# Kernel optimization log

Measured on AMD Instinct MI355X. Metric: run time of the kernel, lower is better.

The kernel has to match this reference:

```python
import jax, jax.numpy as jnp
import numpy as np


def _rms(x, w=None, eps=1e-6):
    # RMSNorm in fp32 like the torch module, optional elementwise affine.
    x32 = x.astype(jnp.float32)
    r = jax.lax.rsqrt(jnp.mean(x32 * x32, axis=-1, keepdims=True) + eps)
    y = (x32 * r).astype(x.dtype)
    return y * w if w is not None else y


def _rotate_half(x):
    x1, x2 = jnp.split(x, 2, axis=-1)
    return jnp.concatenate([-x2, x1], axis=-1)


def setup_inputs() -> dict:
    key = jax.random.key(0)
    ks = jax.random.split(key, 10)
    B, N, C, H = 16, 1024, 1152, 16
    hd = C // H          # 72
    hid = 3072           # _swiglu_hidden(1152, 4.0)
    grid = 32            # grid**2 == N
    quarter = hd // 4    # 18
    # exact axial RoPE cache (build_axial_rope_cache)
    inv_freq = 1.0 / (10000.0 ** (np.arange(quarter, dtype=np.float32) / quarter))
    pos = np.arange(grid, dtype=np.float32)
    f1 = pos[:, None] * inv_freq[None, :]                               # (grid, quarter)
    fy = np.broadcast_to(f1[:, None, :], (grid, grid, quarter)).reshape(-1, quarter)
    fx = np.broadcast_to(f1[None, :, :], (grid, grid, quarter)).reshape(-1, quarter)

    def cs(f):
        e = np.concatenate([f, f], axis=-1)                             # (N, hd//2)
        return jnp.asarray(np.cos(e))[None, None], jnp.asarray(np.sin(e))[None, None]

    cos_y, sin_y = cs(fy)
    cos_x, sin_x = cs(fx)

    def w(k, shp, scale=0.02):
        return jax.random.normal(k, shp, jnp.float32) * scale

    return {
        "x": jax.random.normal(ks[0], (B, N, C), jnp.float32),
        "temb": jax.random.normal(ks[1], (B, C), jnp.float32),
        "cos_y": cos_y, "sin_y": sin_y, "cos_x": cos_x, "sin_x": sin_x,
        "Wqkv": w(ks[2], (3 * C, C)), "bqkv": jnp.zeros((3 * C,), jnp.float32),
        "Wt": w(ks[3], (3 * C, C)), "bt": jnp.zeros((3 * C,), jnp.float32),
        "Wp": w(ks[4], (C, C)), "bp": jnp.zeros((C,), jnp.float32),
        "qn_w": jnp.ones((hd,), jnp.float32), "kn_w": jnp.ones((hd,), jnp.float32),
        "Wg": w(ks[5], (hid, C)), "bg": jnp.zeros((hid,), jnp.float32),
        "Wu": w(ks[6], (hid, C)), "bu": jnp.zeros((hid,), jnp.float32),
        "Wd": w(ks[7], (C, hid)), "bd": jnp.zeros((C,), jnp.float32),
    }


def reference(x, temb, cos_y, sin_y, cos_x, sin_x, Wqkv, bqkv, Wt, bt, Wp, bp,
              qn_w, kn_w, Wg, bg, Wu, bu, Wd, bd):
    B, N, C = x.shape
    H = 16
    hd = C // H

    # --- TMSA attention branch ---
    xn = _rms(x)                                            # norm1 (no affine)
    qkv = xn @ Wqkv.T + bqkv + (temb @ Wt.T + bt)[:, None, :]
    qkv = qkv.reshape(B, N, 3, H, hd).transpose(2, 0, 3, 1, 4)  # (3,B,H,N,hd)
    q, k, v = qkv[0], qkv[1], qkv[2]
    q = _rms(q, qn_w)
    k = _rms(k, kn_w)

    def rope(t):
        ty, tx = jnp.split(t, 2, axis=-1)
        ty = ty * cos_y + _rotate_half(ty) * sin_y
        tx = tx * cos_x + _rotate_half(tx) * sin_x
        return jnp.concatenate([ty, tx], axis=-1)

    q, k = rope(q), rope(k)

    scores = jnp.einsum('bhnd,bhmd->bhnm', q, k) / jnp.sqrt(jnp.float32(hd))
    attn = jax.nn.softmax(scores, axis=-1)
    o = jnp.einsum('bhnm,bhmd->bhnd', attn, v)
    o = o.transpose(0, 2, 1, 3).reshape(B, N, C)
    x = x + (o @ Wp.T + bp)

    # --- SwiGLU MLP branch ---
    xn2 = _rms(x)                                           # norm2 (no affine)
    h = jax.nn.silu(xn2 @ Wg.T + bg) * (xn2 @ Wu.T + bu)
    x = x + (h @ Wd.T + bd)
    return x
```

## Files before the change

### kernel.cpp

```cpp
#include <hip/hip_runtime.h>
#include <cstdint>
#include <cstddef>

typedef unsigned short u16;
typedef unsigned int u32;
typedef __attribute__((ext_vector_type(8))) short bf16x8s;
typedef __attribute__((ext_vector_type(4))) float f32x4;

__device__ __forceinline__ u16 f2bf(float f){
  union { float f; unsigned u; } v; v.f = f;
  unsigned r = v.u + 0x7FFFu + ((v.u >> 16) & 1u);
  return (u16)(r >> 16);
}
__device__ __forceinline__ float bf2f(u16 h){
  union { unsigned u; float f; } v; v.u = ((unsigned)h) << 16;
  return v.f;
}

__global__ __launch_bounds__(256) void cvt_kernel(const float* __restrict__ in,
                                                  u16* __restrict__ out, int n){
  int i = blockIdx.x*256 + threadIdx.x;
  if (i < n) out[i] = f2bf(in[i]);
}

__global__ __launch_bounds__(256) void cvt_gu_kernel(const float* __restrict__ Wg,
                                                     const float* __restrict__ Wu,
                                                     u16* __restrict__ out){
  size_t i = (size_t)blockIdx.x*256 + threadIdx.x;
  if (i >= (size_t)6144*1152) return;
  int j = (int)(i / 1152), k = (int)(i % 1152);
  int b16 = j >> 4, w = j & 15;
  int src = (b16 >> 1)*16 + w;
  const float* W = (b16 & 1) ? Wu : Wg;
  out[i] = f2bf(W[(size_t)src*1152 + k]);
}

__global__ __launch_bounds__(256) void temb_kernel(const float* __restrict__ temb,
                                                   const float* __restrict__ Wt,
                                                   const float* __restrict__ bt,
                                                   const float* __restrict__ bqkv,
                                                   float* __restrict__ tvec){
  int idx = blockIdx.x*256 + threadIdx.x;
  if (idx >= 16*3456) return;
  int b = idx / 3456, col = idx % 3456;
  const float* tp = temb + (size_t)b*1152;
  const float* wp = Wt + (size_t)col*1152;
  float s = 0.f;
  for (int k=0;k<1152;k++) s += tp[k]*wp[k];
  tvec[idx] = s + bt[col] + bqkv[col];
}

__global__ __launch_bounds__(256) void rms_kernel(const float* __restrict__ in,
                                                  u16* __restrict__ out, int C){
  int row = blockIdx.x;
  const float* p = in + (size_t)row*C;
  float ss = 0.f;
  for (int c = threadIdx.x; c < C; c += 256){ float v = p[c]; ss += v*v; }
  #pragma unroll
  for (int d=1; d<64; d<<=1) ss += __shfl_xor(ss, d);
  __shared__ float wsum[4];
  if ((threadIdx.x & 63) == 0) wsum[threadIdx.x>>6] = ss;
  __syncthreads();
  float tot = wsum[0]+wsum[1]+wsum[2]+wsum[3];
  float r = rsqrtf(tot/(float)C + 1e-6f);
  u16* o = out + (size_t)row*C;
  for (int c = threadIdx.x; c < C; c += 256) o[c] = f2bf(p[c]*r);
}

template<int MODE>
__global__ __launch_bounds__(256, 3) void gemm_kernel(
    const u16* __restrict__ A, const u16* __restrict__ B,
    int M, int N, int K, int nbx, int segw,
    const float* __restrict__ bias, const float* __restrict__ fextra,
    void* __restrict__ outv, u16* __restrict__ out2, u16* __restrict__ out3)
{
  __shared__ __align__(16) u16 As0[128*32];
  __shared__ __align__(16) u16 Bs0[128*32];
  __shared__ __align__(16) u16 As1[128*32];
  __shared__ __align__(16) u16 Bs1[128*32];
  __shared__ __align__(16) u16 As2[128*32];
  __shared__ __align__(16) u16 Bs2[128*32];
  const int tid  = threadIdx.x;
  const int lane = tid & 63;
  const int wv   = tid >> 6;
  const int wr   = wv >> 1, wc = wv & 1;

  const int nwg  = (int)gridDim.x;
  const int bid  = (int)blockIdx.x;
  const int xcd  = bid & 7;
  const int slot = bid >> 3;
  const int mdep = (nwg >> 3) / nbx;
  const int segsz = mdep * segw;
  const int seg  = slot / segsz;
  const int rem  = slot - seg*segsz;
  const int mi   = rem / segw;
  const int ni   = seg*segw + (rem - mi*segw);
  const long m0 = (long)(xcd*mdep + mi) * 128;
  const long n0 = (long)ni * 128;

  const u16* Ab = A + (size_t)m0*K;
  const u16* Bb = B + (size_t)n0*K;
  const int srow = tid >> 2;
  const int spos = (tid & 3) * 8;

  f32x4 acc[4][4];
  #pragma unroll
  for (int i=0;i<4;i++)
    #pragma unroll
    for (int j=0;j<4;j++) acc[i][j] = (f32x4){0.f,0.f,0.f,0.f};

  auto stage = [&](u16* as, u16* bs, int kt){
    __builtin_amdgcn_global_load_lds(
      (const __attribute__((address_space(1))) void*)(Ab + (size_t)srow*K + kt + spos),
      (__attribute__((address_space(3))) void*)(as + wv*512), 16, 0, 0);
    __builtin_amdgcn_global_load_lds(
      (const __attribute__((address_space(1))) void*)(Ab + (size_t)(64+srow)*K + kt + spos),
      (__attribute__((address_space(3))) void*)(as + 2048 + wv*512), 16, 0, 0);
    __builtin_amdgcn_global_load_lds(
      (const __attribute__((address_space(1))) void*)(Bb + (size_t)srow*K + kt + spos),
      (__attribute__((address_space(3))) void*)(bs + wv*512), 16, 0, 0);
    __builtin_amdgcn_global_load_lds(
      (const __attribute__((address_space(1))) void*)(Bb + (size_t)(64+srow)*K + kt + spos),
      (__attribute__((address_space(3))) void*)(bs + 2048 + wv*512), 16, 0, 0);
  };
  auto compute = [&](const u16* as, const u16* bs){
    const int kb = (lane>>4)*8;
    const int lc = lane & 15;
    bf16x8s af[4], bfr[4];
    #pragma unroll
    for (int i=0;i<4;i++)
      af[i] = *(const bf16x8s*)(as + (wr*64 + i*16 + lc)*32 + kb);
    #pragma unroll
    for (int j=0;j<4;j++)
      bfr[j] = *(const bf16x8s*)(bs + (wc*64 + j*16 + lc)*32 + kb);
    #pragma unroll
    for (int i=0;i<4;i++)
      #pragma unroll
      for (int j=0;j<4;j++)
        acc[i][j] = __builtin_amdgcn_mfma_f32_16x16x32_bf16(af[i], bfr[j], acc[i][j], 0,0,0);
  };

  const int NT = K >> 5;
  stage(As0, Bs0, 0);
  stage(As1, Bs1, 32);
  asm volatile("s_waitcnt vmcnt(4)" ::: "memory");
  __builtin_amdgcn_s_barrier();
  __builtin_amdgcn_sched_barrier(0);

  for (int t = 0; t < NT; t += 3){
    if (t+2 < NT) stage(As2, Bs2, (t+2)*32);
    compute(As0, Bs0);
    if (t+2 < NT) asm volatile("s_waitcnt vmcnt(4)" ::: "memory");
    else          asm volatile("s_waitcnt vmcnt(0)" ::: "memory");
    __builtin_amdgcn_s_barrier();
    __builtin_amdgcn_sched_barrier(0);
    if (t+3 < NT) stage(As0, Bs0, (t+3)*32);
    compute(As1, Bs1);
    if (t+3 < NT) asm volatile("s_waitcnt vmcnt(4)" ::: "memory");
    else          asm volatile("s_waitcnt vmcnt(0)" ::: "memory");
    __builtin_amdgcn_s_barrier();
    __builtin_amdgcn_sched_barrier(0);
    if (t+4 < NT) stage(As1, Bs1, (t+4)*32);
    compute(As2, Bs2);
    if (t+4 < NT) asm volatile("s_waitcnt vmcnt(4)" ::: "memory");
    else          asm volatile("s_waitcnt vmcnt(0)" ::: "memory");
    __builtin_amdgcn_s_barrier();
    __builtin_amdgcn_sched_barrier(0);
  }

  const int lr = (lane>>4)*4, lc = lane&15;
  if (MODE==5){
    #pragma unroll
    for (int i=0;i<4;i++){
      #pragma unroll
      for (int jp=0;jp<2;jp++){
        long hcol = (n0>>1) + wc*32 + jp*16 + lc;
        float bgv = bias[hcol], buv = fextra[hcol];
        #pragma unroll
        for (int r=0;r<4;r++){
          long rowg = m0 + wr*64 + i*16 + lr + r;
          float gv = acc[i][2*jp][r] + bgv;
          float uv = acc[i][2*jp+1][r] + buv;
          float hv = (gv/(1.f + __expf(-gv))) * uv;
          ((u16*)outv)[(size_t)rowg*3072 + hcol] = f2bf(hv);
        }
      }
    }
    return;
  }
  #pragma unroll
  for (int i=0;i<4;i++){
    #pragma unroll
    for (int j=0;j<4;j++){
      long colg = n0 + wc*64 + j*16 + lc;
      long rowg0 = m0 + wr*64 + i*16 + lr;
      if (MODE==0){
        int cg = (int)colg;
        int which = cg / 1152;
        int rem2 = cg - which*1152;
        int hh = rem2 / 72, dd = rem2 - hh*72;
        int b = (int)(rowg0 >> 10), n = (int)(rowg0 & 1023);
        size_t bh = (size_t)(b*16 + hh);
        float tadd = fextra[(size_t)b*3456 + colg];
        if (which == 2){
          ushort4 vv;
          vv.x = f2bf(acc[i][j][0] + tadd);
          vv.y = f2bf(acc[i][j][1] + tadd);
          vv.z = f2bf(acc[i][j][2] + tadd);
          vv.w = f2bf(acc[i][j][3] + tadd);
          *(ushort4*)(out3 + (bh*72 + dd)*1024 + n) = vv;
        } else {
          u16* dst = (which==0) ? (u16*)outv : out2;
          #pragma unroll
          for (int r=0;r<4;r++)
            dst[(bh*1024 + (size_t)(n + r))*72 + dd] = f2bf(acc[i][j][r] + tadd);
        }
      } else {
        #pragma unroll
        for (int r=0;r<4;r++){
          long rowg = rowg0 + r;
          float v = acc[i][j][r];
          size_t oi = (size_t)rowg*N + colg;
          v += bias[colg] + fextra[oi];
          ((float*)outv)[oi] = v;
        }
      }
    }
  }
}

__global__ __launch_bounds__(256) void qkrope_kernel(
    u16* __restrict__ Q, u16* __restrict__ K,
    const float* __restrict__ qn_w, const float* __restrict__ kn_w,
    const float* __restrict__ cos_y, const float* __restrict__ sin_y,
    const float* __restrict__ cos_x, const float* __restrict__ sin_x)
{
  const int gw   = blockIdx.x*4 + (threadIdx.x>>6);
  const int lane = threadIdx.x & 63;
  const int n = gw & 1023;
  const int d0 = lane*2;
  const bool act = d0 < 72;
  const float scale = 0.11785113019775793f;

  u16* qp = Q + (size_t)gw*72;
  u16* kp = K + (size_t)gw*72;
  float q0=0,q1=0,k0=0,k1=0,wq0=0,wq1=0,wk0=0,wk1=0;
  if (act){
    q0 = bf2f(qp[d0]); q1 = bf2f(qp[d0+1]);
    k0 = bf2f(kp[d0]); k1 = bf2f(kp[d0+1]);
    wq0 = qn_w[d0]; wq1 = qn_w[d0+1];
    wk0 = kn_w[d0]; wk1 = kn_w[d0+1];
  }
  float ssq = q0*q0 + q1*q1;
  float ssk = k0*k0 + k1*k1;
  #pragma unroll
  for (int d=1; d<64; d<<=1){ ssq += __shfl_xor(ssq,d); ssk += __shfl_xor(ssk,d); }
  const float rq = rsqrtf(ssq*(1.f/72.f) + 1e-6f);
  const float rk = rsqrtf(ssk*(1.f/72.f) + 1e-6f);
  float qn0 = q0*rq*wq0, qn1 = q1*rq*wq1;
  float kn0 = k0*rk*wk0, kn1 = k1*rk*wk1;

  int dh = d0 % 36;
  const bool first = (dh < 18);
  int partner = first ? lane+9 : lane-9;
  if (!act) partner = lane;
  float pq0 = __shfl(qn0, partner), pq1 = __shfl(qn1, partner);
  float pk0 = __shfl(kn0, partner), pk1 = __shfl(kn1, partner);
  if (act){
    const float* cp = (d0 < 36) ? cos_y : cos_x;
    const float* sp = (d0 < 36) ? sin_y : sin_x;
    float c0 = cp[n*36+dh], c1 = cp[n*36+dh+1];
    float s0 = sp[n*36+dh], s1 = sp[n*36+dh+1];
    float sgn = first ? -1.f : 1.f;
    float qo0 = (qn0*c0 + sgn*pq0*s0)*scale, qo1 = (qn1*c1 + sgn*pq1*s1)*scale;
    float ko0 = kn0*c0 + sgn*pk0*s0,         ko1 = kn1*c1 + sgn*pk1*s1;
    *(unsigned*)(qp + d0) = (unsigned)f2bf(qo0) | ((unsigned)f2bf(qo1)<<16);
    *(unsigned*)(kp + d0) = (unsigned)f2bf(ko0) | ((unsigned)f2bf(ko1)<<16);
  }
}

__global__ __launch_bounds__(256, 3) void attn_kernel(
    const u16* __restrict__ Q, const u16* __restrict__ K,
    const u16* __restrict__ Vt, u16* __restrict__ O)
{
  const int tid  = threadIdx.x;
  const int lane = tid & 63;
  const int wv   = tid >> 6;
  const int g = lane >> 4, c = lane & 15;
  const int bid  = blockIdx.x;
  const int head = (bid >> 6) * 8 + (bid & 7);
  const int q0   = ((bid >> 3) & 7) * 128;
  const int b = head >> 4, h = head & 15;

  __shared__ __align__(16) u16 Vlds[80][72];
  __shared__ __align__(16) u16 Plds[8][16][64];

  const bf16x8s zf = {0,0,0,0,0,0,0,0};
  const u16* Kp = K + (size_t)head*1024*72;
  const u16* Qb = Q + ((size_t)head*1024 + q0 + wv*32)*72;
  const char* Vg = (const char*)(Vt + (size_t)head*72*1024);

  bf16x8s qf[2][3];
  #pragma unroll
  for (int s=0;s<2;s++){
    const u16* qrow = Qb + (size_t)(s*16 + c)*72;
    qf[s][0] = *(const bf16x8s*)(qrow + g*8);
    qf[s][1] = *(const bf16x8s*)(qrow + 32 + g*8);
    qf[s][2] = (g==0) ? *(const bf16x8s*)(qrow + 64) : zf;
  }

  f32x4 oacc[2][5];
  float lsum[2] = {0.f, 0.f};
  #pragma unroll
  for (int s=0;s<2;s++)
    #pragma unroll
    for (int c5=0;c5<5;c5++) oacc[s][c5] = (f32x4){0.f,0.f,0.f,0.f};

  char* pb0 = (char*)Plds + (wv*2+0)*2048 + c*128;
  char* pb1 = pb0 + 2048;
  const int swz = (c & 7) << 4;

  int4 vr0, vr1, vr2;
  {
    vr0 = *(const int4*)(Vg + ((tid    )>>3)*2048 + ((tid    )&7)*16);
    vr1 = *(const int4*)(Vg + ((256+tid)>>3)*2048 + ((256+tid)&7)*16);
    if (tid < 64) vr2 = *(const int4*)(Vg + ((512+tid)>>3)*2048 + ((512+tid)&7)*16);
  }
  if (tid < 288) ((u32*)&Vlds[72][0])[tid] = 0u;
  {
    *(int4*)((char*)Vlds + ((tid    )>>3)*144 + ((tid    )&7)*16) = vr0;
    *(int4*)((char*)Vlds + ((256+tid)>>3)*144 + ((256+tid)&7)*16) = vr1;
    if (tid < 64) *(int4*)((char*)Vlds + ((512+tid)>>3)*144 + ((512+tid)&7)*16) = vr2;
  }

  for (int t = 0; t < 16; ++t){
    const int kv0 = t*64;
    __syncthreads();
    if (t < 15){
      const char* vs = Vg + (kv0+64)*2;
      vr0 = *(const int4*)(vs + ((tid    )>>3)*2048 + ((tid    )&7)*16);
      vr1 = *(const int4*)(vs + ((256+tid)>>3)*2048 + ((256+tid)&7)*16);
      if (tid < 64) vr2 = *(const int4*)(vs + ((512+tid)>>3)*2048 + ((512+tid)&7)*16);
    }

    #pragma unroll
    for (int nf=0; nf<4; nf++){
      const u16* krow = Kp + (size_t)(kv0 + nf*16 + c)*72;
      bf16x8s kf0 = *(const bf16x8s*)(krow + g*8);
      bf16x8s kf1 = *(const bf16x8s*)(krow + 32 + g*8);
      bf16x8s kf2 = (g==0) ? *(const bf16x8s*)(krow + 64) : zf;
      #pragma unroll
      for (int s=0;s<2;s++){
        f32x4 sc = (f32x4){0.f,0.f,0.f,0.f};
        sc = __builtin_amdgcn_mfma_f32_16x16x32_bf16(kf0, qf[s][0], sc,0,0,0);
        sc = __builtin_amdgcn_mfma_f32_16x16x32_bf16(kf1, qf[s][1], sc,0,0,0);
        sc = __builtin_amdgcn_mfma_f32_16x16x32_bf16(kf2, qf[s][2], sc,0,0,0);
        float p0 = __expf(sc[0]), p1 = __expf(sc[1]);
        float p2 = __expf(sc[2]), p3 = __expf(sc[3]);
        lsum[s] += (p0+p1) + (p2+p3);
        u32 w0 = (u32)f2bf(p0) | ((u32)f2bf(p1) << 16);
        u32 w1 = (u32)f2bf(p2) | ((u32)f2bf(p3) << 16);
        char* pb = s ? pb1 : pb0;
        int kb = nf*32 + g*8;
        *(u32*)(pb + ( kb      ^ swz)) = w0;
        *(u32*)(pb + ((kb + 4) ^ swz)) = w1;
      }
    }
    asm volatile("" ::: "memory");
    bf16x8s pa[2][2];
    #pragma unroll
    for (int s=0;s<2;s++)
      #pragma unroll
      for (int w2=0;w2<2;w2++)
        pa[s][w2] = *(const bf16x8s*)((s?pb1:pb0) + ((w2*64 + g*16) ^ swz));

    #pragma unroll
    for (int c5=0;c5<5;c5++){
      #pragma unroll
      for (int w2=0;w2<2;w2++){
        bf16x8s vf = *(const bf16x8s*)((const char*)Vlds + (size_t)(c5*16+c)*144 + w2*64 + g*16);
        oacc[0][c5] = __builtin_amdgcn_mfma_f32_16x16x32_bf16(pa[0][w2], vf, oacc[0][c5],0,0,0);
        oacc[1][c5] = __builtin_amdgcn_mfma_f32_16x16x32_bf16(pa[1][w2], vf, oacc[1][c5],0,0,0);
      }
    }

    if (t < 15){
      __syncthreads();
      *(int4*)((char*)Vlds + ((tid    )>>3)*144 + ((tid    )&7)*16) = vr0;
      *(int4*)((char*)Vlds + ((256+tid)>>3)*144 + ((256+tid)&7)*16) = vr1;
      if (tid < 64) *(int4*)((char*)Vlds + ((512+tid)>>3)*144 + ((512+tid)&7)*16) = vr2;
    }
  }

  size_t obase = (size_t)b*1024*1152 + (size_t)h*72;
  #pragma unroll
  for (int s=0;s<2;s++){
    float ls = lsum[s];
    ls += __shfl_xor(ls, 16);
    ls += __shfl_xor(ls, 32);
    float linv[4];
    #pragma unroll
    for (int r=0;r<4;r++) linv[r] = 1.0f / __shfl(ls, 4*g + r);
    #pragma unroll
    for (int c5=0;c5<5;c5++){
      int d = c5*16 + c;
      if (d < 72){
        #pragma unroll
        for (int r=0;r<4;r++){
          int n = q0 + wv*32 + s*16 + 4*g + r;
          O[obase + (size_t)n*1152 + d] = f2bf(oacc[s][c5][r]*linv[r]);
        }
      }
    }
  }
}

extern "C" void kernel_launch(void* const* d_in, const int* in_sizes, int n_in,
                              void* d_out, int out_size, void* d_ws, size_t ws_size,
                              hipStream_t stream) {
  const float* x    = (const float*)d_in[0];
  const float* temb = (const float*)d_in[1];
  const float* cos_y= (const float*)d_in[2];
  const float* sin_y= (const float*)d_in[3];
  const float* cos_x= (const float*)d_in[4];
  const float* sin_x= (const float*)d_in[5];
  const float* Wqkv = (const float*)d_in[6];
  const float* bqkv = (const float*)d_in[7];
  const float* Wt   = (const float*)d_in[8];
  const float* bt   = (const float*)d_in[9];
  const float* Wp   = (const float*)d_in[10];
  const float* bp   = (const float*)d_in[11];
  const float* qn_w = (const float*)d_in[12];
  const float* kn_w = (const float*)d_in[13];
  const float* Wg   = (const float*)d_in[14];
  const float* bg   = (const float*)d_in[15];
  const float* Wu   = (const float*)d_in[16];
  const float* bu   = (const float*)d_in[17];
  const float* Wd   = (const float*)d_in[18];
  const float* bd   = (const float*)d_in[19];

  char* ws = (char*)d_ws;
  size_t off = 0;
  auto alloc = [&](size_t bytes)->void*{
    off = (off + 255) & ~(size_t)255;
    void* p = ws + off; off += bytes; return p;
  };

  u16*   wbuf  = (u16*)alloc((size_t)6144*1152*2);
  float* tvec  = (float*)alloc((size_t)16*3456*4);
  u16*   xn_bf = (u16*)alloc((size_t)16384*1152*2);
  u16*   qt    = (u16*)alloc((size_t)262144*72*2);
  u16*   kt    = (u16*)alloc((size_t)262144*72*2);
  u16*   vt    = (u16*)alloc((size_t)256*72*1024*2);
  if (off > ws_size) return;

  u16*   o_bf   = xn_bf;
  u16*   xn2_bf = xn_bf;
  u16*   gbuf   = qt;
  float* x1     = (float*)d_out;

  rms_kernel<<<16384,256,0,stream>>>(x, xn_bf, 1152);
  temb_kernel<<<(16*3456+255)/256,256,0,stream>>>(temb, Wt, bt, bqkv, tvec);

  cvt_kernel<<<(3456*1152+255)/256,256,0,stream>>>(Wqkv, wbuf, 3456*1152);
  gemm_kernel<0><<<27*128,256,0,stream>>>(
      xn_bf, wbuf, 16384, 3456, 1152, 27, 9, nullptr, tvec, qt, kt, vt);

  qkrope_kernel<<<65536,256,0,stream>>>(qt, kt, qn_w, kn_w, cos_y, sin_y, cos_x, sin_x);

  attn_kernel<<<2048,256,0,stream>>>(qt, kt, vt, o_bf);

  cvt_kernel<<<(1152*1152+255)/256,256,0,stream>>>(Wp, wbuf, 1152*1152);
  gemm_kernel<1><<<9*128,256,0,stream>>>(
      o_bf, wbuf, 16384, 1152, 1152, 9, 9, bp, x, x1, nullptr, nullptr);

  rms_kernel<<<16384,256,0,stream>>>(x1, xn2_bf, 1152);

  cvt_gu_kernel<<<(6144*1152+255)/256,256,0,stream>>>(Wg, Wu, wbuf);
  gemm_kernel<5><<<48*128,256,0,stream>>>(
      xn2_bf, wbuf, 16384, 6144, 1152, 48, 8, bg, bu, gbuf, nullptr, nullptr);

  cvt_kernel<<<(1152*3072+255)/256,256,0,stream>>>(Wd, wbuf, 1152*3072);
  gemm_kernel<4><<<9*128,256,0,stream>>>(
      gbuf, wbuf, 16384, 1152, 3072, 9, 3, bd, x1, (float*)d_out, nullptr, nullptr);
}
```

Measured before the change: 1.007 ms.

## Enlarge GEMM tiles to 256x128 with 8 waves, swizzle LDS, rewrite temb GEMV

The bf16 MFMA GEMM now computes a 256x128 output tile per 512-thread block (8 waves, each 64x64) instead of 128x128 with 4 waves. Each B tile is reused across twice as many rows, which cuts global and L2 traffic per flop. Staging loads now XOR-swizzle the K chunk per row so the LDS fragment reads avoid bank conflicts, and the vmcnt waits shrink to match the three loads per stage. The temb projection is rewritten to give one wavefront per output column, reading the weight row once and reducing over all 16 batches with shuffles. The trade-offs are larger LDS use per block (about 73 KB with triple buffering) and fewer blocks per GEMM, which may lower occupancy and hurt tail balance.

```diff
diff --git a/kernel.cpp b/kernel.cpp
--- a/kernel.cpp
+++ b/kernel.cpp
@@ -40,14 +40,31 @@
                                                    const float* __restrict__ bt,
                                                    const float* __restrict__ bqkv,
                                                    float* __restrict__ tvec){
-  int idx = blockIdx.x*256 + threadIdx.x;
-  if (idx >= 16*3456) return;
-  int b = idx / 3456, col = idx % 3456;
-  const float* tp = temb + (size_t)b*1152;
+  const int col  = blockIdx.x*4 + (threadIdx.x>>6);
+  const int lane = threadIdx.x & 63;
   const float* wp = Wt + (size_t)col*1152;
-  float s = 0.f;
-  for (int k=0;k<1152;k++) s += tp[k]*wp[k];
-  tvec[idx] = s + bt[col] + bqkv[col];
+  float w[18];
+  #pragma unroll
+  for (int j=0;j<18;j++) w[j] = wp[lane + j*64];
+  float acc[16];
+  #pragma unroll
+  for (int b=0;b<16;b++) acc[b] = 0.f;
+  #pragma unroll
+  for (int j=0;j<18;j++){
+    const int k = lane + j*64;
+    #pragma unroll
+    for (int b=0;b<16;b++) acc[b] += w[j]*temb[b*1152 + k];
+  }
+  #pragma unroll
+  for (int b=0;b<16;b++){
+    #pragma unroll
+    for (int d=1; d<64; d<<=1) acc[b] += __shfl_xor(acc[b], d);
+  }
+  if (lane == 0){
+    float add = bt[col] + bqkv[col];
+    #pragma unroll
+    for (int b=0;b<16;b++) tvec[(size_t)b*3456 + col] = acc[b] + add;
+  }
 }
 
 __global__ __launch_bounds__(256) void rms_kernel(const float* __restrict__ in,
@@ -68,17 +85,17 @@
 }
 
 template<int MODE>
-__global__ __launch_bounds__(256, 3) void gemm_kernel(
+__global__ __launch_bounds__(512, 4) void gemm_kernel(
     const u16* __restrict__ A, const u16* __restrict__ B,
     int M, int N, int K, int nbx, int segw,
     const float* __restrict__ bias, const float* __restrict__ fextra,
     void* __restrict__ outv, u16* __restrict__ out2, u16* __restrict__ out3)
 {
-  __shared__ __align__(16) u16 As0[128*32];
+  __shared__ __align__(16) u16 As0[256*32];
+  __shared__ __align__(16) u16 As1[256*32];
+  __shared__ __align__(16) u16 As2[256*32];
   __shared__ __align__(16) u16 Bs0[128*32];
-  __shared__ __align__(16) u16 As1[128*32];
   __shared__ __align__(16) u16 Bs1[128*32];
-  __shared__ __align__(16) u16 As2[128*32];
   __shared__ __align__(16) u16 Bs2[128*32];
   const int tid  = threadIdx.x;
   const int lane = tid & 63;
@@ -95,13 +112,14 @@
   const int rem  = slot - seg*segsz;
   const int mi   = rem / segw;
   const int ni   = seg*segw + (rem - mi*segw);
-  const long m0 = (long)(xcd*mdep + mi) * 128;
+  const long m0 = (long)(xcd*mdep + mi) * 256;
   const long n0 = (long)ni * 128;
 
   const u16* Ab = A + (size_t)m0*K;
   const u16* Bb = B + (size_t)n0*K;
-  const int srow = tid >> 2;
-  const int spos = (tid & 3) * 8;
+
+  const int gsw  = ((lane&3) ^ ((lane>>3)&3)) * 8;
+  const int srow = lane >> 2;
 
   f32x4 acc[4][4];
   #pragma unroll
@@ -111,28 +129,25 @@
 
   auto stage = [&](u16* as, u16* bs, int kt){
     __builtin_amdgcn_global_load_lds(
-      (const __attribute__((address_space(1))) void*)(Ab + (size_t)srow*K + kt + spos),
+      (const __attribute__((address_space(1))) void*)(Ab + (size_t)(wv*16 + srow)*K + kt + gsw),
       (__attribute__((address_space(3))) void*)(as + wv*512), 16, 0, 0);
     __builtin_amdgcn_global_load_lds(
-      (const __attribute__((address_space(1))) void*)(Ab + (size_t)(64+srow)*K + kt + spos),
-      (__attribute__((address_space(3))) void*)(as + 2048 + wv*512), 16, 0, 0);
+      (const __attribute__((address_space(1))) void*)(Ab + (size_t)(128 + wv*16 + srow)*K + kt + gsw),
+      (__attribute__((address_space(3))) void*)(as + 4096 + wv*512), 16, 0, 0);
     __builtin_amdgcn_global_load_lds(
-      (const __attribute__((address_space(1))) void*)(Bb + (size_t)srow*K + kt + spos),
+      (const __attribute__((address_space(1))) void*)(Bb + (size_t)(wv*16 + srow)*K + kt + gsw),
       (__attribute__((address_space(3))) void*)(bs + wv*512), 16, 0, 0);
-    __builtin_amdgcn_global_load_lds(
-      (const __attribute__((address_space(1))) void*)(Bb + (size_t)(64+srow)*K + kt + spos),
-      (__attribute__((address_space(3))) void*)(bs + 2048 + wv*512), 16, 0, 0);
   };
   auto compute = [&](const u16* as, const u16* bs){
-    const int kb = (lane>>4)*8;
-    const int lc = lane & 15;
+    const int swc = (((lane>>4) ^ ((lane>>1)&3))) * 8;
+    const int lc16 = lane & 15;
     bf16x8s af[4], bfr[4];
     #pragma unroll
     for (int i=0;i<4;i++)
-      af[i] = *(const bf16x8s*)(as + (wr*64 + i*16 + lc)*32 + kb);
+      af[i] = *(const bf16x8s*)(as + (wr*64 + i*16 + lc16)*32 + swc);
     #pragma unroll
     for (int j=0;j<4;j++)
-      bfr[j] = *(const bf16x8s*)(bs + (wc*64 + j*16 + lc)*32 + kb);
+      bfr[j] = *(const bf16x8s*)(bs + (wc*64 + j*16 + lc16)*32 + swc);
     #pragma unroll
     for (int i=0;i<4;i++)
       #pragma unroll
@@ -143,26 +158,26 @@
   const int NT = K >> 5;
   stage(As0, Bs0, 0);
   stage(As1, Bs1, 32);
-  asm volatile("s_waitcnt vmcnt(4)" ::: "memory");
+  asm volatile("s_waitcnt vmcnt(3)" ::: "memory");
   __builtin_amdgcn_s_barrier();
   __builtin_amdgcn_sched_barrier(0);
 
   for (int t = 0; t < NT; t += 3){
     if (t+2 < NT) stage(As2, Bs2, (t+2)*32);
     compute(As0, Bs0);
-    if (t+2 < NT) asm volatile("s_waitcnt vmcnt(4)" ::: "memory");
+    if (t+2 < NT) asm volatile("s_waitcnt vmcnt(3)" ::: "memory");
     else          asm volatile("s_waitcnt vmcnt(0)" ::: "memory");
     __builtin_amdgcn_s_barrier();
     __builtin_amdgcn_sched_barrier(0);
     if (t+3 < NT) stage(As0, Bs0, (t+3)*32);
     compute(As1, Bs1);
-    if (t+3 < NT) asm volatile("s_waitcnt vmcnt(4)" ::: "memory");
+    if (t+3 < NT) asm volatile("s_waitcnt vmcnt(3)" ::: "memory");
     else          asm volatile("s_waitcnt vmcnt(0)" ::: "memory");
     __builtin_amdgcn_s_barrier();
     __builtin_amdgcn_sched_barrier(0);
     if (t+4 < NT) stage(As1, Bs1, (t+4)*32);
     compute(As2, Bs2);
-    if (t+4 < NT) asm volatile("s_waitcnt vmcnt(4)" ::: "memory");
+    if (t+4 < NT) asm volatile("s_waitcnt vmcnt(3)" ::: "memory");
     else          asm volatile("s_waitcnt vmcnt(0)" ::: "memory");
     __builtin_amdgcn_s_barrier();
     __builtin_amdgcn_sched_barrier(0);
@@ -460,10 +475,10 @@
   float* x1     = (float*)d_out;
 
   rms_kernel<<<16384,256,0,stream>>>(x, xn_bf, 1152);
-  temb_kernel<<<(16*3456+255)/256,256,0,stream>>>(temb, Wt, bt, bqkv, tvec);
+  temb_kernel<<<864,256,0,stream>>>(temb, Wt, bt, bqkv, tvec);
 
   cvt_kernel<<<(3456*1152+255)/256,256,0,stream>>>(Wqkv, wbuf, 3456*1152);
-  gemm_kernel<0><<<27*128,256,0,stream>>>(
+  gemm_kernel<0><<<64*27,512,0,stream>>>(
       xn_bf, wbuf, 16384, 3456, 1152, 27, 9, nullptr, tvec, qt, kt, vt);
 
   qkrope_kernel<<<65536,256,0,stream>>>(qt, kt, qn_w, kn_w, cos_y, sin_y, cos_x, sin_x);
@@ -471,16 +486,16 @@
   attn_kernel<<<2048,256,0,stream>>>(qt, kt, vt, o_bf);
 
   cvt_kernel<<<(1152*1152+255)/256,256,0,stream>>>(Wp, wbuf, 1152*1152);
-  gemm_kernel<1><<<9*128,256,0,stream>>>(
+  gemm_kernel<1><<<64*9,512,0,stream>>>(
       o_bf, wbuf, 16384, 1152, 1152, 9, 9, bp, x, x1, nullptr, nullptr);
 
   rms_kernel<<<16384,256,0,stream>>>(x1, xn2_bf, 1152);
 
   cvt_gu_kernel<<<(6144*1152+255)/256,256,0,stream>>>(Wg, Wu, wbuf);
-  gemm_kernel<5><<<48*128,256,0,stream>>>(
+  gemm_kernel<5><<<64*48,512,0,stream>>>(
       xn2_bf, wbuf, 16384, 6144, 1152, 48, 8, bg, bu, gbuf, nullptr, nullptr);
 
   cvt_kernel<<<(1152*3072+255)/256,256,0,stream>>>(Wd, wbuf, 1152*3072);
-  gemm_kernel<4><<<9*128,256,0,stream>>>(
+  gemm_kernel<4><<<64*9,512,0,stream>>>(
       gbuf, wbuf, 16384, 1152, 3072, 9, 3, bd, x1, (float*)d_out, nullptr, nullptr);
 }
```

New measurement: 1.020 ms. Within noise of the previous version (+1.3%).
